# Performance work log

Measured on AMD Instinct MI355X. Metric: run time of the kernel, lower is better.

The kernel has to match this reference:

```python
import jax, jax.numpy as jnp
import numpy as np

B = 4096
N_COL = 100      # all-numerical columns
N_COND = 64      # d*m = 4*16
D = 4
TOTAL = N_COL * N_COND   # 6400
N_RODT = TOTAL // D      # 1600
N_EST = 160              # max(2,int(sqrt(100))) * N_COND // D
N_FOREST = 100
N_HIDDEN = 128
N_CLASS = 10
EPS = 1e-5


def group_norm(x, w, b, groups):
    # x: [B, C] (spatial dim of 1 dropped); normalize within each channel group
    Bn, C = x.shape
    xg = x.reshape(Bn, groups, C // groups)
    mu = xg.mean(-1, keepdims=True)
    var = ((xg - mu) ** 2).mean(-1, keepdims=True)
    xn = ((xg - mu) * jax.lax.rsqrt(var + EPS)).reshape(Bn, C)
    return xn * w + b


def layer_norm(x, w, b):
    mu = x.mean(-1, keepdims=True)
    var = ((x - mu) ** 2).mean(-1, keepdims=True)
    return (x - mu) * jax.lax.rsqrt(var + EPS) * w + b


def setup_inputs() -> dict:
    key = jax.random.key(0)
    ks = jax.random.split(key, 16)
    s = 0.3  # weight scale
    x = jax.random.normal(ks[0], (B, N_COL), jnp.float32)
    w1 = jax.random.normal(ks[1], (N_COL, N_COND), jnp.float32) * s
    b1 = jax.random.normal(ks[2], (N_COL, N_COND), jnp.float32) * s
    perm = jax.random.permutation(ks[3], TOTAL)
    gn1_w = jnp.ones((TOTAL,), jnp.float32)
    gn1_b = jnp.zeros((TOTAL,), jnp.float32)
    conv2_w = jax.random.normal(ks[4], (N_RODT, D, D), jnp.float32) * s
    conv2_b = jax.random.normal(ks[5], (TOTAL,), jnp.float32) * s
    gn2_w = jnp.ones((TOTAL,), jnp.float32)
    gn2_b = jnp.zeros((TOTAL,), jnp.float32)
    conv3_w = jax.random.normal(ks[6], (N_RODT, D, 1), jnp.float32) * s
    conv3_b = jax.random.normal(ks[7], (N_RODT,), jnp.float32) * s
    # sample-without-replacement per forest (eval-mode fixed indices)
    swr = jax.vmap(lambda k: jax.random.permutation(k, N_RODT)[:N_EST])(
        jax.random.split(ks[8], N_FOREST))
    E = jax.random.normal(ks[9], (N_RODT, N_HIDDEN), jnp.float32)
    ln1_w = jnp.ones((N_HIDDEN,), jnp.float32)
    ln1_b = jnp.zeros((N_HIDDEN,), jnp.float32)
    fc1_w = jax.random.normal(ks[10], (N_HIDDEN, N_HIDDEN), jnp.float32) * (1.0 / np.sqrt(N_HIDDEN))
    fc1_b = jnp.zeros((N_HIDDEN,), jnp.float32)
    ln2_w = jnp.ones((N_HIDDEN,), jnp.float32)
    ln2_b = jnp.zeros((N_HIDDEN,), jnp.float32)
    fc2_w = jax.random.normal(ks[11], (N_HIDDEN, N_CLASS), jnp.float32) * (1.0 / np.sqrt(N_HIDDEN))
    fc2_b = jnp.zeros((N_CLASS,), jnp.float32)
    return dict(x=x, w1=w1, b1=b1, perm=perm, gn1_w=gn1_w, gn1_b=gn1_b,
                conv2_w=conv2_w, conv2_b=conv2_b, gn2_w=gn2_w, gn2_b=gn2_b,
                conv3_w=conv3_w, conv3_b=conv3_b, swr=swr, E=E,
                ln1_w=ln1_w, ln1_b=ln1_b, fc1_w=fc1_w, fc1_b=fc1_b,
                ln2_w=ln2_w, ln2_b=ln2_b, fc2_w=fc2_w, fc2_b=fc2_b)


def reference(x, w1, b1, perm, gn1_w, gn1_b, conv2_w, conv2_b, gn2_w, gn2_b,
              conv3_w, conv3_b, swr, E, ln1_w, ln1_b, fc1_w, fc1_b,
              ln2_w, ln2_b, fc2_w, fc2_b):
    b = x.shape[0]
    # --- ConditionGeneration (numerical path): per-column 1->n_cond group conv + sigmoid
    M = jax.nn.sigmoid(x[:, :, None] * w1[None] + b1[None])        # [B, n_col, n_cond]
    M = M.transpose(0, 2, 1)                                        # [B, n_cond, n_col]
    # --- rODTConstruction: flatten + fixed permutation
    O = M.reshape(b, -1)[:, perm]                                   # [B, total]
    # --- phi_2: GN -> grouped 4->4 conv -> ReLU -> GN -> grouped 4->1 conv
    h = group_norm(O, gn1_w, gn1_b, N_RODT)
    h = jnp.einsum('bgi,gio->bgo', h.reshape(b, N_RODT, D), conv2_w).reshape(b, TOTAL) + conv2_b
    h = jax.nn.relu(h)
    h = group_norm(h, gn2_w, gn2_b, N_RODT)
    w = jnp.einsum('bgi,gio->bgo', h.reshape(b, N_RODT, D), conv3_w)[..., 0] + conv3_b  # [B, n_rodt] (n_head=1)
    # --- rODT forest: gather estimators, softmax over estimators, weighted sum of rODT embeddings
    ws = jax.nn.softmax(w[:, swr], axis=2)                          # [B, n_forest, n_est]
    Ep = E[swr]                                                     # [n_forest, n_est, n_hidden]
    F = jnp.einsum('bfe,fed->bfd', ws, Ep)                          # [B, n_forest, n_hidden]
    # --- bagging MLP (dropout=0)
    h2 = layer_norm(F, ln1_w, ln1_b)
    h2 = jax.nn.relu(h2 @ fc1_w + fc1_b)
    h2 = layer_norm(h2, ln2_w, ln2_b)
    y_hat = h2 @ fc2_w + fc2_b                                      # [B, n_forest, n_class]
    return y_hat.mean(1)                                            # [B, n_class]
```

## Files before the change

kernel.cpp:

```cpp
#include <hip/hip_runtime.h>
#include <hip/hip_bf16.h>
#include <stdint.h>

#define NB 4096
#define NCOL 100
#define NCOND 64
#define NTOTAL 6400
#define NRODT 1600
#define NEST 160
#define NFOR 100
#define NHID 128
#define NCLS 10
#define GEPS 1e-5f

typedef __attribute__((ext_vector_type(8))) short short8;
typedef __attribute__((ext_vector_type(4))) float floatx4;

__device__ __forceinline__ unsigned f2bfu(float x) {
  union { float f; unsigned u; } v; v.f = x;
  return (v.u + 0x8000u) >> 16;
}
__device__ __forceinline__ float bf2f(unsigned short u) {
  union { unsigned u; float f; } v; v.u = ((unsigned)u) << 16;
  return v.f;
}

__device__ __forceinline__ float rowsum16(float v) {
  union { float f; int i; } a, t;
  a.f = v;
  t.i = __builtin_amdgcn_update_dpp(0, a.i, 0x128, 0xf, 0xf, true); a.f += t.f;
  t.i = __builtin_amdgcn_update_dpp(0, a.i, 0x124, 0xf, 0xf, true); a.f += t.f;
  t.i = __builtin_amdgcn_update_dpp(0, a.i, 0x122, 0xf, 0xf, true); a.f += t.f;
  t.i = __builtin_amdgcn_update_dpp(0, a.i, 0x121, 0xf, 0xf, true); a.f += t.f;
  return a.f;
}

__global__ __launch_bounds__(256) void k01_prep(
    const float* __restrict__ x, const float* __restrict__ w1,
    const float* __restrict__ b1, const int* __restrict__ perm,
    const float* __restrict__ gn1w, const float* __restrict__ gn1b,
    const float* __restrict__ c2w, const float* __restrict__ c2b,
    const float* __restrict__ gn2w, const float* __restrict__ gn2b,
    const float* __restrict__ c3w, const float* __restrict__ c3b,
    const float* __restrict__ E, const int* __restrict__ swr,
    const float* __restrict__ fc1w, const float* __restrict__ fc2w,
    unsigned short* __restrict__ wT,
    unsigned short* __restrict__ Bf, unsigned short* __restrict__ W1f,
    unsigned short* __restrict__ W2f, float* __restrict__ out)
{
  __shared__ float xl[64 * NCOL];
  __shared__ int ridx[NEST];
  const int tid = threadIdx.x;
  const int blk = blockIdx.x;

  if (blk < 1600) {
    const int b0 = (blk & 63) * 64;
    const int g  = (blk >> 6) * 64 + (tid >> 2);
    const int i4 = tid & 3;
    for (int i = tid; i < 64 * NCOL; i += 256)
      xl[i] = x[(size_t)b0 * NCOL + i];
    __syncthreads();

    const int4 p4 = *(const int4*)(perm + 4 * g);
    const int pv[4] = {p4.x, p4.y, p4.z, p4.w};
    float w1v[4], b1v[4];
    int pc[4];
#pragma unroll
    for (int i = 0; i < 4; i++) {
      unsigned p = (unsigned)pv[i];
      unsigned j = p / 100u;
      unsigned cc = p - j * 100u;
      pc[i] = (int)cc;
      w1v[i] = w1[cc * NCOND + j];
      b1v[i] = b1[cc * NCOND + j];
    }
    const float4 g1w = *(const float4*)(gn1w + 4 * g);
    const float4 g1b = *(const float4*)(gn1b + 4 * g);
    const float4 cw0 = *(const float4*)(c2w + 16 * g);
    const float4 cw1 = *(const float4*)(c2w + 16 * g + 4);
    const float4 cw2 = *(const float4*)(c2w + 16 * g + 8);
    const float4 cw3 = *(const float4*)(c2w + 16 * g + 12);
    const float4 cbv = *(const float4*)(c2b + 4 * g);
    const float4 g2w = *(const float4*)(gn2w + 4 * g);
    const float4 g2b = *(const float4*)(gn2b + 4 * g);
    const float4 c3v = *(const float4*)(c3w + 4 * g);
    const float c3bv = c3b[g];

    for (int k = 0; k < 4; k++) {
      float v4[4];
#pragma unroll
      for (int j = 0; j < 4; j++) {
        const int bb = k * 16 + i4 * 4 + j;
        float O[4];
#pragma unroll
        for (int i = 0; i < 4; i++) {
          float a = xl[bb * NCOL + pc[i]] * w1v[i] + b1v[i];
          O[i] = 1.0f / (1.0f + __expf(-a));
        }
        float mu = 0.25f * (O[0] + O[1] + O[2] + O[3]);
        float d[4], var = 0.f;
#pragma unroll
        for (int i = 0; i < 4; i++) { d[i] = O[i] - mu; var += d[i] * d[i]; }
        float rs = rsqrtf(0.25f * var + GEPS);
        float xn0 = d[0] * rs * g1w.x + g1b.x;
        float xn1 = d[1] * rs * g1w.y + g1b.y;
        float xn2 = d[2] * rs * g1w.z + g1b.z;
        float xn3 = d[3] * rs * g1w.w + g1b.w;
        float h[4];
        h[0] = xn0*cw0.x + xn1*cw1.x + xn2*cw2.x + xn3*cw3.x + cbv.x;
        h[1] = xn0*cw0.y + xn1*cw1.y + xn2*cw2.y + xn3*cw3.y + cbv.y;
        h[2] = xn0*cw0.z + xn1*cw1.z + xn2*cw2.z + xn3*cw3.z + cbv.z;
        h[3] = xn0*cw0.w + xn1*cw1.w + xn2*cw2.w + xn3*cw3.w + cbv.w;
#pragma unroll
        for (int i = 0; i < 4; i++) h[i] = fmaxf(h[i], 0.f);
        float mu2 = 0.25f * (h[0] + h[1] + h[2] + h[3]);
        float e[4], var2 = 0.f;
#pragma unroll
        for (int i = 0; i < 4; i++) { e[i] = h[i] - mu2; var2 += e[i] * e[i]; }
        float rs2 = rsqrtf(0.25f * var2 + GEPS);
        float hn0 = e[0] * rs2 * g2w.x + g2b.x;
        float hn1 = e[1] * rs2 * g2w.y + g2b.y;
        float hn2 = e[2] * rs2 * g2w.z + g2b.z;
        float hn3 = e[3] * rs2 * g2w.w + g2b.w;
        v4[j] = hn0*c3v.x + hn1*c3v.y + hn2*c3v.z + hn3*c3v.w + c3bv;
      }
      uint2 pk;
      pk.x = f2bfu(__expf(v4[0])) | (f2bfu(__expf(v4[1])) << 16);
      pk.y = f2bfu(__expf(v4[2])) | (f2bfu(__expf(v4[3])) << 16);
      *(uint2*)(wT + (size_t)g * NB + b0 + k * 16 + i4 * 4) = pk;
    }
  } else if (blk < 1600 + NFOR) {
    const int fblk = blk - 1600;
    if (tid < NEST) ridx[tid] = swr[fblk * NEST + tid];
    __syncthreads();
    for (int m = tid; m < 2560; m += 256) {
      int lane = m & 63, rest = m >> 6;
      int kc = rest % 5, n = rest / 5;
      int q = lane >> 4, c = lane & 15;
      int e0 = kc * 32 + q * 8;
      int h = n * 16 + c;
      union { unsigned short v[8]; uint4 u; } t;
#pragma unroll
      for (int j = 0; j < 8; j++)
        t.v[j] = (unsigned short)f2bfu(E[(size_t)ridx[e0 + j] * NHID + h]);
      *(uint4*)(Bf + (size_t)fblk * 20480 + (size_t)m * 8) = t.u;
    }
  } else if (blk == 1600 + NFOR) {
    for (int m = tid; m < 2048; m += 256) {
      int lane = m & 63, rest = m >> 6;
      int kc = rest & 3, n = rest >> 2;
      int q = lane >> 4, c = lane & 15;
      int k0 = kc * 32 + q * 8;
      int o = n * 16 + c;
      union { unsigned short v[8]; uint4 u; } t;
#pragma unroll
      for (int j = 0; j < 8; j++)
        t.v[j] = (unsigned short)f2bfu(fc1w[(size_t)(k0 + j) * NHID + o]);
      *(uint4*)(W1f + (size_t)m * 8) = t.u;
    }
  } else if (blk == 1601 + NFOR) {
    for (int m = tid; m < 256; m += 256) {
      int lane = m & 63, kc = m >> 6;
      int q = lane >> 4, c = lane & 15;
      int k0 = kc * 32 + q * 8;
      union { unsigned short v[8]; uint4 u; } t;
#pragma unroll
      for (int j = 0; j < 8; j++)
        t.v[j] = (unsigned short)f2bfu(c < NCLS ? fc2w[(size_t)(k0 + j) * NCLS + c] : 0.f);
      *(uint4*)(W2f + (size_t)m * 8) = t.u;
    }
  } else {
    const int z = blk - (1602 + NFOR);
    float4 zz = make_float4(0.f, 0.f, 0.f, 0.f);
    for (int i = z * 256 + tid; i < NB * NCLS / 4; i += 3 * 256)
      ((float4*)out)[i] = zz;
  }
}

__global__ __launch_bounds__(256, 3) void k3_mfma(
    const unsigned short* __restrict__ wT,
    const int* __restrict__ swr,
    const unsigned short* __restrict__ Bf,
    const unsigned short* __restrict__ W1f,
    const unsigned short* __restrict__ W2f,
    const float* __restrict__ ln1w, const float* __restrict__ ln1b,
    const float* __restrict__ fc1b,
    const float* __restrict__ ln2w, const float* __restrict__ ln2b,
    const float* __restrict__ fc2b,
    float* __restrict__ out)
{
  __shared__ unsigned short lsA[128 * 168];
  __shared__ __align__(16) float sPT[128][4];

  const int tid = threadIdx.x;
  const int b0 = blockIdx.x * 128;
  const int f  = blockIdx.y;
  const int lane = tid & 63;
  const int wv = __builtin_amdgcn_readfirstlane(tid >> 6);
  const int c = lane & 15, q = lane >> 4;

  {
    const unsigned short* wbase = wT + b0 + lane;
    const int* swf = swr + f * NEST + wv * 40;
    float ssum0 = 0.f, ssum1 = 0.f;
#pragma unroll
    for (int k = 0; k < 5; k++) {
      int id8[8];
#pragma unroll
      for (int jj = 0; jj < 8; jj++) id8[jj] = swf[k * 8 + jj];
      unsigned short us0[8], us1[8];
#pragma unroll
      for (int jj = 0; jj < 8; jj++) {
        const unsigned short* p = wbase + (size_t)id8[jj] * NB;
        us0[jj] = p[0];
        us1[jj] = p[64];
        ssum0 += bf2f(us0[jj]);
        ssum1 += bf2f(us1[jj]);
      }
      uint4 pk0 = {(unsigned)us0[0] | ((unsigned)us0[1] << 16),
                   (unsigned)us0[2] | ((unsigned)us0[3] << 16),
                   (unsigned)us0[4] | ((unsigned)us0[5] << 16),
                   (unsigned)us0[6] | ((unsigned)us0[7] << 16)};
      uint4 pk1 = {(unsigned)us1[0] | ((unsigned)us1[1] << 16),
                   (unsigned)us1[2] | ((unsigned)us1[3] << 16),
                   (unsigned)us1[4] | ((unsigned)us1[5] << 16),
                   (unsigned)us1[6] | ((unsigned)us1[7] << 16)};
      *(uint4*)(lsA + lane * 168 + wv * 40 + k * 8) = pk0;
      *(uint4*)(lsA + (64 + lane) * 168 + wv * 40 + k * 8) = pk1;
    }
    sPT[lane][wv] = ssum0;
    sPT[64 + lane][wv] = ssum1;
  }
  __syncthreads();

  const unsigned short* pa0 = lsA + (wv * 16 + c) * 168 + q * 8;
  const unsigned short* pa1 = pa0 + 64 * 168;
  floatx4 acc0[8], acc1[8];
#pragma unroll
  for (int n = 0; n < 8; n++) {
    acc0[n] = (floatx4){0.f, 0.f, 0.f, 0.f};
    acc1[n] = (floatx4){0.f, 0.f, 0.f, 0.f};
  }
  const unsigned short* bbase = Bf + (size_t)f * 20480 + lane * 8;
#pragma unroll
  for (int kc = 0; kc < 5; kc++) {
    short8 a0 = *(const short8*)(pa0 + kc * 32);
    short8 a1 = *(const short8*)(pa1 + kc * 32);
#pragma unroll
    for (int n = 0; n < 8; n++) {
      short8 b = *(const short8*)(bbase + n * 2560 + kc * 512);
      acc0[n] = __builtin_amdgcn_mfma_f32_16x16x32_bf16(a0, b, acc0[n], 0, 0, 0);
      acc1[n] = __builtin_amdgcn_mfma_f32_16x16x32_bf16(a1, b, acc1[n], 0, 0, 0);
    }
  }

  {
    float lw[8], lb[8];
#pragma unroll
    for (int n = 0; n < 8; n++) { lw[n] = ln1w[n * 16 + c]; lb[n] = ln1b[n * 16 + c]; }
#pragma unroll
    for (int rr = 0; rr < 4; rr++) {
      const int row = wv * 16 + q * 4 + rr;
      {
        const float4 sv = *(const float4*)&sPT[row][0];
        float st = sv.x + sv.y + sv.z + sv.w;
        float s1 = 0.f, s2 = 0.f;
#pragma unroll
        for (int n = 0; n < 8; n++) { float v = acc0[n][rr]; s1 += v; s2 += v * v; }
        s1 = rowsum16(s1);
        s2 = rowsum16(s2);
        float mu = s1 * (1.f / 128.f);
        float var = fmaxf(s2 * (1.f / 128.f) - mu * mu, 0.f);
        float rs = rsqrtf(var + GEPS * st * st);
#pragma unroll
        for (int n = 0; n < 8; n++)
          acc0[n][rr] = (acc0[n][rr] - mu) * rs * lw[n] + lb[n];
      }
      {
        const float4 sv = *(const float4*)&sPT[64 + row][0];
        float st = sv.x + sv.y + sv.z + sv.w;
        float s1 = 0.f, s2 = 0.f;
#pragma unroll
        for (int n = 0; n < 8; n++) { float v = acc1[n][rr]; s1 += v; s2 += v * v; }
        s1 = rowsum16(s1);
        s2 = rowsum16(s2);
        float mu = s1 * (1.f / 128.f);
        float var = fmaxf(s2 * (1.f / 128.f) - mu * mu, 0.f);
        float rs = rsqrtf(var + GEPS * st * st);
#pragma unroll
        for (int n = 0; n < 8; n++)
          acc1[n][rr] = (acc1[n][rr] - mu) * rs * lw[n] + lb[n];
      }
    }
  }

#pragma unroll
  for (int rr = 0; rr < 4; rr++)
#pragma unroll
    for (int n = 0; n < 8; n++) {
      lsA[(wv * 16 + q * 4 + rr) * 168 + n * 16 + c] =
          (unsigned short)f2bfu(acc0[n][rr]);
      lsA[(64 + wv * 16 + q * 4 + rr) * 168 + n * 16 + c] =
          (unsigned short)f2bfu(acc1[n][rr]);
    }

  {
    short8 a00 = *(const short8*)(pa0);
    short8 a01 = *(const short8*)(pa0 + 32);
    short8 a02 = *(const short8*)(pa0 + 64);
    short8 a03 = *(const short8*)(pa0 + 96);
    short8 a10 = *(const short8*)(pa1);
    short8 a11 = *(const short8*)(pa1 + 32);
    short8 a12 = *(const short8*)(pa1 + 64);
    short8 a13 = *(const short8*)(pa1 + 96);
    const unsigned short* w1p = W1f + lane * 8;
#pragma unroll
    for (int n = 0; n < 8; n++) {
      const unsigned short* wp = w1p + n * 2048;
      short8 b0v = *(const short8*)(wp);
      short8 b1v = *(const short8*)(wp + 512);
      short8 b2v = *(const short8*)(wp + 1024);
      short8 b3v = *(const short8*)(wp + 1536);
      floatx4 t0 = __builtin_amdgcn_mfma_f32_16x16x32_bf16(a00, b0v, (floatx4){0.f,0.f,0.f,0.f}, 0, 0, 0);
      t0 = __builtin_amdgcn_mfma_f32_16x16x32_bf16(a01, b1v, t0, 0, 0, 0);
      t0 = __builtin_amdgcn_mfma_f32_16x16x32_bf16(a02, b2v, t0, 0, 0, 0);
      t0 = __builtin_amdgcn_mfma_f32_16x16x32_bf16(a03, b3v, t0, 0, 0, 0);
      floatx4 t1 = __builtin_amdgcn_mfma_f32_16x16x32_bf16(a10, b0v, (floatx4){0.f,0.f,0.f,0.f}, 0, 0, 0);
      t1 = __builtin_amdgcn_mfma_f32_16x16x32_bf16(a11, b1v, t1, 0, 0, 0);
      t1 = __builtin_amdgcn_mfma_f32_16x16x32_bf16(a12, b2v, t1, 0, 0, 0);
      t1 = __builtin_amdgcn_mfma_f32_16x16x32_bf16(a13, b3v, t1, 0, 0, 0);
      acc0[n] = t0;
      acc1[n] = t1;
    }
  }

  {
    float fb[8], lw[8], lb[8];
#pragma unroll
    for (int n = 0; n < 8; n++) {
      fb[n] = fc1b[n * 16 + c];
      lw[n] = ln2w[n * 16 + c]; lb[n] = ln2b[n * 16 + c];
    }
#pragma unroll
    for (int rr = 0; rr < 4; rr++) {
      {
#pragma unroll
        for (int n = 0; n < 8; n++) acc0[n][rr] = fmaxf(acc0[n][rr] + fb[n], 0.f);
        float s1 = 0.f, s2 = 0.f;
#pragma unroll
        for (int n = 0; n < 8; n++) { float v = acc0[n][rr]; s1 += v; s2 += v * v; }
        s1 = rowsum16(s1);
        s2 = rowsum16(s2);
        float mu = s1 * (1.f / 128.f);
        float var = fmaxf(s2 * (1.f / 128.f) - mu * mu, 0.f);
        float rs = rsqrtf(var + GEPS);
#pragma unroll
        for (int n = 0; n < 8; n++)
          acc0[n][rr] = (acc0[n][rr] - mu) * rs * lw[n] + lb[n];
      }
      {
#pragma unroll
        for (int n = 0; n < 8; n++) acc1[n][rr] = fmaxf(acc1[n][rr] + fb[n], 0.f);
        float s1 = 0.f, s2 = 0.f;
#pragma unroll
        for (int n = 0; n < 8; n++) { float v = acc1[n][rr]; s1 += v; s2 += v * v; }
        s1 = rowsum16(s1);
        s2 = rowsum16(s2);
        float mu = s1 * (1.f / 128.f);
        float var = fmaxf(s2 * (1.f / 128.f) - mu * mu, 0.f);
        float rs = rsqrtf(var + GEPS);
#pragma unroll
        for (int n = 0; n < 8; n++)
          acc1[n][rr] = (acc1[n][rr] - mu) * rs * lw[n] + lb[n];
      }
    }
  }

#pragma unroll
  for (int rr = 0; rr < 4; rr++)
#pragma unroll
    for (int n = 0; n < 8; n++) {
      lsA[(wv * 16 + q * 4 + rr) * 168 + n * 16 + c] =
          (unsigned short)f2bfu(acc0[n][rr]);
      lsA[(64 + wv * 16 + q * 4 + rr) * 168 + n * 16 + c] =
          (unsigned short)f2bfu(acc1[n][rr]);
    }

  floatx4 o40 = (floatx4){0.f, 0.f, 0.f, 0.f};
  floatx4 o41 = (floatx4){0.f, 0.f, 0.f, 0.f};
#pragma unroll
  for (int kc = 0; kc < 4; kc++) {
    short8 a0 = *(const short8*)(pa0 + kc * 32);
    short8 a1 = *(const short8*)(pa1 + kc * 32);
    short8 b = *(const short8*)(W2f + kc * 512 + lane * 8);
    o40 = __builtin_amdgcn_mfma_f32_16x16x32_bf16(a0, b, o40, 0, 0, 0);
    o41 = __builtin_amdgcn_mfma_f32_16x16x32_bf16(a1, b, o41, 0, 0, 0);
  }
  if (c < NCLS) {
    float bias = fc2b[c];
#pragma unroll
    for (int rr = 0; rr < 4; rr++) {
      atomicAdd(out + (size_t)(b0 + wv * 16 + q * 4 + rr) * NCLS + c,
                (o40[rr] + bias) * 0.01f);
      atomicAdd(out + (size_t)(b0 + 64 + wv * 16 + q * 4 + rr) * NCLS + c,
                (o41[rr] + bias) * 0.01f);
    }
  }
}

extern "C" void kernel_launch(void* const* d_in, const int* in_sizes, int n_in,
                              void* d_out, int out_size, void* d_ws, size_t ws_size,
                              hipStream_t stream)
{
  (void)in_sizes; (void)n_in; (void)ws_size; (void)out_size;
  const float* x    = (const float*)d_in[0];
  const float* w1   = (const float*)d_in[1];
  const float* b1   = (const float*)d_in[2];
  const int*   perm = (const int*)d_in[3];
  const float* gn1w = (const float*)d_in[4];
  const float* gn1b = (const float*)d_in[5];
  const float* c2w  = (const float*)d_in[6];
  const float* c2b  = (const float*)d_in[7];
  const float* gn2w = (const float*)d_in[8];
  const float* gn2b = (const float*)d_in[9];
  const float* c3w  = (const float*)d_in[10];
  const float* c3b  = (const float*)d_in[11];
  const int*   swr  = (const int*)d_in[12];
  const float* E    = (const float*)d_in[13];
  const float* ln1w = (const float*)d_in[14];
  const float* ln1b = (const float*)d_in[15];
  const float* fc1w = (const float*)d_in[16];
  const float* fc1b = (const float*)d_in[17];
  const float* ln2w = (const float*)d_in[18];
  const float* ln2b = (const float*)d_in[19];
  const float* fc2w = (const float*)d_in[20];
  const float* fc2b = (const float*)d_in[21];
  float* out = (float*)d_out;

  const size_t W_BYTES = (size_t)NB * NRODT * 2;
  unsigned short* wTbuf = (unsigned short*)d_ws;
  unsigned short* Bfb   = (unsigned short*)((char*)d_ws + W_BYTES);
  unsigned short* W1fb  = (unsigned short*)((char*)d_ws + W_BYTES + 4096000);
  unsigned short* W2fb  = (unsigned short*)((char*)d_ws + W_BYTES + 4096000 + 32768);

  k01_prep<<<1600 + NFOR + 2 + 3, 256, 0, stream>>>(
      x, w1, b1, perm, gn1w, gn1b, c2w, c2b, gn2w, gn2b, c3w, c3b,
      E, swr, fc1w, fc2w, wTbuf, Bfb, W1fb, W2fb, out);
  dim3 g3(NB / 128, NFOR);
  k3_mfma<<<g3, 256, 0, stream>>>(wTbuf, swr, Bfb, W1fb, W2fb,
                                  ln1w, ln1b, fc1b, ln2w, ln2b, fc2b, out);
}
```

Before: 211.1 us.

## Compute softmax row sums via MFMA with ones vector and batch gather loads

```diff
diff --git a/kernel.cpp b/kernel.cpp
--- a/kernel.cpp
+++ b/kernel.cpp
@@ -32,6 +32,12 @@
   t.i = __builtin_amdgcn_update_dpp(0, a.i, 0x124, 0xf, 0xf, true); a.f += t.f;
   t.i = __builtin_amdgcn_update_dpp(0, a.i, 0x122, 0xf, 0xf, true); a.f += t.f;
   t.i = __builtin_amdgcn_update_dpp(0, a.i, 0x121, 0xf, 0xf, true); a.f += t.f;
+  return a.f;
+}
+
+__device__ __forceinline__ float bcast16(float v) {
+  union { float f; int i; } a; a.f = v;
+  a.i = __builtin_amdgcn_ds_swizzle(a.i, 0x0010);
   return a.f;
 }
 
@@ -190,7 +196,6 @@
     float* __restrict__ out)
 {
   __shared__ unsigned short lsA[128 * 168];
-  __shared__ __align__(16) float sPT[128][4];
 
   const int tid = threadIdx.x;
   const int b0 = blockIdx.x * 128;
@@ -202,48 +207,77 @@
   {
     const unsigned short* wbase = wT + b0 + lane;
     const int* swf = swr + f * NEST + wv * 40;
-    float ssum0 = 0.f, ssum1 = 0.f;
-#pragma unroll
-    for (int k = 0; k < 5; k++) {
-      int id8[8];
-#pragma unroll
-      for (int jj = 0; jj < 8; jj++) id8[jj] = swf[k * 8 + jj];
-      unsigned short us0[8], us1[8];
-#pragma unroll
-      for (int jj = 0; jj < 8; jj++) {
-        const unsigned short* p = wbase + (size_t)id8[jj] * NB;
-        us0[jj] = p[0];
-        us1[jj] = p[64];
-        ssum0 += bf2f(us0[jj]);
-        ssum1 += bf2f(us1[jj]);
-      }
-      uint4 pk0 = {(unsigned)us0[0] | ((unsigned)us0[1] << 16),
-                   (unsigned)us0[2] | ((unsigned)us0[3] << 16),
-                   (unsigned)us0[4] | ((unsigned)us0[5] << 16),
-                   (unsigned)us0[6] | ((unsigned)us0[7] << 16)};
-      uint4 pk1 = {(unsigned)us1[0] | ((unsigned)us1[1] << 16),
-                   (unsigned)us1[2] | ((unsigned)us1[3] << 16),
-                   (unsigned)us1[4] | ((unsigned)us1[5] << 16),
-                   (unsigned)us1[6] | ((unsigned)us1[7] << 16)};
-      *(uint4*)(lsA + lane * 168 + wv * 40 + k * 8) = pk0;
-      *(uint4*)(lsA + (64 + lane) * 168 + wv * 40 + k * 8) = pk1;
-    }
-    sPT[lane][wv] = ssum0;
-    sPT[64 + lane][wv] = ssum1;
-  }
+    int idx[40];
+#pragma unroll
+    for (int e = 0; e < 40; e++) idx[e] = swf[e];
+
+    unsigned short* r0 = lsA + lane * 168 + wv * 40;
+    unsigned short* r1 = r0 + 64 * 168;
+
+#pragma unroll
+    for (int h = 0; h < 2; h++) {
+      unsigned short u0[20], u1[20];
+#pragma unroll
+      for (int e = 0; e < 20; e++) {
+        const unsigned short* p = wbase + (size_t)idx[h * 20 + e] * NB;
+        u0[e] = p[0];
+        u1[e] = p[64];
+      }
+#define MKU(a, i) ((unsigned)(a)[i] | ((unsigned)(a)[i + 1] << 16))
+      if (h == 0) {
+        uint4 a0 = {MKU(u0,0), MKU(u0,2), MKU(u0,4), MKU(u0,6)};
+        uint4 b0v = {MKU(u0,8), MKU(u0,10), MKU(u0,12), MKU(u0,14)};
+        uint2 c0 = {MKU(u0,16), MKU(u0,18)};
+        *(uint4*)(r0 + 0) = a0;  *(uint4*)(r0 + 8) = b0v;  *(uint2*)(r0 + 16) = c0;
+        uint4 a1 = {MKU(u1,0), MKU(u1,2), MKU(u1,4), MKU(u1,6)};
+        uint4 b1v = {MKU(u1,8), MKU(u1,10), MKU(u1,12), MKU(u1,14)};
+        uint2 c1 = {MKU(u1,16), MKU(u1,18)};
+        *(uint4*)(r1 + 0) = a1;  *(uint4*)(r1 + 8) = b1v;  *(uint2*)(r1 + 16) = c1;
+      } else {
+        uint2 a0 = {MKU(u0,0), MKU(u0,2)};
+        uint4 b0v = {MKU(u0,4), MKU(u0,6), MKU(u0,8), MKU(u0,10)};
+        uint4 c0 = {MKU(u0,12), MKU(u0,14), MKU(u0,16), MKU(u0,18)};
+        *(uint2*)(r0 + 20) = a0;  *(uint4*)(r0 + 24) = b0v;  *(uint4*)(r0 + 32) = c0;
+        uint2 a1 = {MKU(u1,0), MKU(u1,2)};
+        uint4 b1v = {MKU(u1,4), MKU(u1,6), MKU(u1,8), MKU(u1,10)};
+        uint4 c1 = {MKU(u1,12), MKU(u1,14), MKU(u1,16), MKU(u1,18)};
+        *(uint2*)(r1 + 20) = a1;  *(uint4*)(r1 + 24) = b1v;  *(uint4*)(r1 + 32) = c1;
+      }
+#undef MKU
+    }
+  }
+
+  const unsigned short* bbase = Bf + (size_t)f * 20480 + lane * 8;
+  short8 bp[8];
+#pragma unroll
+  for (int n = 0; n < 8; n++)
+    bp[n] = *(const short8*)(bbase + n * 2560);
+
   __syncthreads();
 
   const unsigned short* pa0 = lsA + (wv * 16 + c) * 168 + q * 8;
   const unsigned short* pa1 = pa0 + 64 * 168;
+  const short onev = (c == 0) ? (short)0x3F80 : (short)0;
+  short8 bones;
+#pragma unroll
+  for (int j = 0; j < 8; j++) bones[j] = onev;
+
   floatx4 acc0[8], acc1[8];
-#pragma unroll
-  for (int n = 0; n < 8; n++) {
-    acc0[n] = (floatx4){0.f, 0.f, 0.f, 0.f};
-    acc1[n] = (floatx4){0.f, 0.f, 0.f, 0.f};
-  }
-  const unsigned short* bbase = Bf + (size_t)f * 20480 + lane * 8;
-#pragma unroll
-  for (int kc = 0; kc < 5; kc++) {
+  floatx4 accs0 = (floatx4){0.f, 0.f, 0.f, 0.f};
+  floatx4 accs1 = (floatx4){0.f, 0.f, 0.f, 0.f};
+  {
+    short8 a0 = *(const short8*)(pa0);
+    short8 a1 = *(const short8*)(pa1);
+#pragma unroll
+    for (int n = 0; n < 8; n++) {
+      acc0[n] = __builtin_amdgcn_mfma_f32_16x16x32_bf16(a0, bp[n], (floatx4){0.f,0.f,0.f,0.f}, 0, 0, 0);
+      acc1[n] = __builtin_amdgcn_mfma_f32_16x16x32_bf16(a1, bp[n], (floatx4){0.f,0.f,0.f,0.f}, 0, 0, 0);
+    }
+    accs0 = __builtin_amdgcn_mfma_f32_16x16x32_bf16(a0, bones, accs0, 0, 0, 0);
+    accs1 = __builtin_amdgcn_mfma_f32_16x16x32_bf16(a1, bones, accs1, 0, 0, 0);
+  }
+#pragma unroll
+  for (int kc = 1; kc < 5; kc++) {
     short8 a0 = *(const short8*)(pa0 + kc * 32);
     short8 a1 = *(const short8*)(pa1 + kc * 32);
 #pragma unroll
@@ -252,6 +286,8 @@
       acc0[n] = __builtin_amdgcn_mfma_f32_16x16x32_bf16(a0, b, acc0[n], 0, 0, 0);
       acc1[n] = __builtin_amdgcn_mfma_f32_16x16x32_bf16(a1, b, acc1[n], 0, 0, 0);
     }
+    accs0 = __builtin_amdgcn_mfma_f32_16x16x32_bf16(a0, bones, accs0, 0, 0, 0);
+    accs1 = __builtin_amdgcn_mfma_f32_16x16x32_bf16(a1, bones, accs1, 0, 0, 0);
   }
 
   {
@@ -260,10 +296,8 @@
     for (int n = 0; n < 8; n++) { lw[n] = ln1w[n * 16 + c]; lb[n] = ln1b[n * 16 + c]; }
 #pragma unroll
     for (int rr = 0; rr < 4; rr++) {
-      const int row = wv * 16 + q * 4 + rr;
       {
-        const float4 sv = *(const float4*)&sPT[row][0];
-        float st = sv.x + sv.y + sv.z + sv.w;
+        float st = bcast16(accs0[rr]);
         float s1 = 0.f, s2 = 0.f;
 #pragma unroll
         for (int n = 0; n < 8; n++) { float v = acc0[n][rr]; s1 += v; s2 += v * v; }
@@ -277,8 +311,7 @@
           acc0[n][rr] = (acc0[n][rr] - mu) * rs * lw[n] + lb[n];
       }
       {
-        const float4 sv = *(const float4*)&sPT[64 + row][0];
-        float st = sv.x + sv.y + sv.z + sv.w;
+        float st = bcast16(accs1[rr]);
         float s1 = 0.f, s2 = 0.f;
 #pragma unroll
         for (int n = 0; n < 8; n++) { float v = acc1[n][rr]; s1 += v; s2 += v * v; }
```

New measurement: 209.3 us. No clear change (-0.9%).
